# Kernel optimization log

Measured on AMD Instinct MI355X. Metric: run time of the kernel, lower is better.

Reference implementation:

```python
import jax, jax.numpy as jnp
import numpy as np

EPS = 1e-6

def rmsnorm(x, w):
    # x * rsqrt(mean(x^2, -1) + eps) * w
    ms = jnp.mean(jnp.square(x), axis=-1, keepdims=True)
    return w * (x * jax.lax.rsqrt(ms + EPS))

def setup_inputs() -> dict:
    key = jax.random.key(0)
    ks = jax.random.split(key, 10)
    B, L, T, D, R = 4, 8, 2048, 1024, 64
    h_base = jax.random.normal(ks[0], (B, T, D), dtype=jnp.float32)
    prev_states = jax.random.normal(ks[1], (B, L, T, D), dtype=jnp.float32)
    query = jax.random.normal(ks[2], (D,), dtype=jnp.float32) * 0.02
    gate = jnp.float32(0.5)
    score_w = jnp.ones((D,), dtype=jnp.float32)
    out_w = jnp.ones((D,), dtype=jnp.float32)
    qnorm_w = jnp.ones((D,), dtype=jnp.float32)
    # low-rank query projections (nn.Linear weight layout: [out, in])
    Wd = jax.random.normal(ks[3], (R, D), dtype=jnp.float32) * 0.02
    Wu = jax.random.normal(ks[4], (D, R), dtype=jnp.float32) * 0.02
    # token gate projection
    tg_w = jax.random.normal(ks[5], (1, D), dtype=jnp.float32) * 0.02
    tg_b = jnp.zeros((1,), dtype=jnp.float32)
    return {"h_base": h_base, "prev_states": prev_states, "query": query,
            "gate": gate, "score_w": score_w, "out_w": out_w,
            "qnorm_w": qnorm_w, "Wd": Wd, "Wu": Wu, "tg_w": tg_w, "tg_b": tg_b}

def reference(h_base, prev_states, query, gate, score_w, out_w, qnorm_w, Wd, Wu, tg_w, tg_b):
    sources = prev_states                              # [B,L,T,D]
    normed = rmsnorm(sources, score_w)                 # [B,L,T,D]
    # low-rank input-dependent query: q = query + up(down(qnorm(h)))
    qh = rmsnorm(h_base, qnorm_w)                      # [B,T,D]
    q = query + jnp.einsum('btr,dr->btd', jnp.einsum('btd,rd->btr', qh, Wd), Wu)
    scores = jnp.einsum('btd,bltd->blt', q, normed)    # [B,L,T]
    alpha = jax.nn.softmax(scores, axis=1)             # softmax over depth L
    delta = jnp.einsum('blt,bltd->btd', alpha, sources)
    delta = rmsnorm(delta, out_w)                      # [B,T,D]
    g = gate * jax.nn.sigmoid(h_base @ tg_w.T + tg_b)  # [B,T,1]
    out = h_base + g * delta
    return out, alpha
```

## Files before the change

### kernel.cpp

```cpp
#include <hip/hip_runtime.h>
#include <hip/hip_bf16.h>

#define D_DIM 1024
#define L_DIM 8
#define T_DIM 2048
#define B_DIM 4
#define TOKS  (B_DIM * T_DIM)
#define OUT_ELEMS ((size_t)TOKS * D_DIM)
#define EPSF 1e-6f

typedef __attribute__((ext_vector_type(8)))  short short8_t;
typedef __attribute__((ext_vector_type(16))) float f32x16_t;

__device__ __forceinline__ float wave_sum(float v) {
#pragma unroll
    for (int off = 32; off; off >>= 1) v += __shfl_xor(v, off, 64);
    return v;
}

__device__ __forceinline__ float dot4(const float4& a, const float4& b) {
    return a.x * b.x + a.y * b.y + a.z * b.z + a.w * b.w;
}

__device__ __forceinline__ unsigned short f2bf(float f) {
    union { __hip_bfloat16 h; unsigned short u; } x;
    x.h = __float2bfloat16(f);
    return x.u;
}

__device__ __forceinline__ float bf2f(unsigned short u) {
    union { unsigned int i; float f; } x;
    x.i = ((unsigned int)u) << 16;
    return x.f;
}

__global__ __launch_bounds__(256) void k_prep(const float* __restrict__ Wd,
                                              const float* __restrict__ qnw,
                                              const float* __restrict__ Wu,
                                              unsigned short* __restrict__ Wdq,
                                              unsigned short* __restrict__ Wubf) {
    int i = (blockIdx.x * 256 + threadIdx.x) * 4;
    float4 wd = *(const float4*)(Wd + i);
    float4 nv = *(const float4*)(qnw + (i & (D_DIM - 1)));
    short4 o1 = make_short4((short)f2bf(wd.x * nv.x), (short)f2bf(wd.y * nv.y),
                            (short)f2bf(wd.z * nv.z), (short)f2bf(wd.w * nv.w));
    *(short4*)(Wdq + i) = o1;
    float4 wu = *(const float4*)(Wu + i);
    short4 o2 = make_short4((short)f2bf(wu.x), (short)f2bf(wu.y),
                            (short)f2bf(wu.z), (short)f2bf(wu.w));
    *(short4*)(Wubf + i) = o2;
}

__global__ __launch_bounds__(512) void k_q(const float* __restrict__ h,
                                           const unsigned short* __restrict__ Wdq,
                                           const unsigned short* __restrict__ Wubf,
                                           const float* __restrict__ query,
                                           const float* __restrict__ score_w,
                                           unsigned short* __restrict__ qs) {
    __shared__ float c_red[8][2][16][64];
    __shared__ float ssq_red[8][32];
    __shared__ float scale_sh[32];
    __shared__ unsigned short r_sw[32 * 64];

    int tid  = threadIdx.x;
    int w    = tid >> 6;
    int lane = tid & 63;
    int t0   = blockIdx.x * 32;

    f32x16_t acc0, acc1;
#pragma unroll
    for (int r = 0; r < 16; ++r) { acc0[r] = 0.f; acc1[r] = 0.f; }

    int arow = lane & 31;
    int koff = w * 128 + (lane >> 5) * 8;
    const float* hrow = h + (size_t)(t0 + arow) * D_DIM + koff;
    const unsigned short* b0 = Wdq + (size_t)arow * D_DIM + koff;
    const unsigned short* b1 = Wdq + (size_t)(32 + arow) * D_DIM + koff;

    float ssq = 0.f;
#pragma unroll
    for (int s = 0; s < 8; ++s) {
        float4 ha = *(const float4*)(hrow + s * 16);
        float4 hb = *(const float4*)(hrow + s * 16 + 4);
        ssq += dot4(ha, ha) + dot4(hb, hb);
        short8_t af;
        af[0] = (short)f2bf(ha.x); af[1] = (short)f2bf(ha.y);
        af[2] = (short)f2bf(ha.z); af[3] = (short)f2bf(ha.w);
        af[4] = (short)f2bf(hb.x); af[5] = (short)f2bf(hb.y);
        af[6] = (short)f2bf(hb.z); af[7] = (short)f2bf(hb.w);
        short8_t bf0 = *(const short8_t*)(b0 + s * 16);
        short8_t bf1 = *(const short8_t*)(b1 + s * 16);
        acc0 = __builtin_amdgcn_mfma_f32_32x32x16_bf16(af, bf0, acc0, 0, 0, 0);
        acc1 = __builtin_amdgcn_mfma_f32_32x32x16_bf16(af, bf1, acc1, 0, 0, 0);
    }

    ssq += __shfl_xor(ssq, 32, 64);
    if (lane < 32) ssq_red[w][lane] = ssq;
#pragma unroll
    for (int r = 0; r < 16; ++r) {
        c_red[w][0][r][lane] = acc0[r];
        c_red[w][1][r][lane] = acc1[r];
    }
    __syncthreads();

    if (tid < 32) {
        float s8 = 0.f;
#pragma unroll
        for (int u = 0; u < 8; ++u) s8 += ssq_red[u][tid];
        scale_sh[tid] = rsqrtf(s8 * (1.f / D_DIM) + EPSF);
    }
    __syncthreads();

    for (int idx = tid; idx < 2048; idx += 512) {
        int nj = idx >> 10, rem = idx & 1023, reg = rem >> 6, ln = rem & 63;
        float v = 0.f;
#pragma unroll
        for (int u = 0; u < 8; ++u) v += c_red[u][nj][reg][ln];
        int tk = (reg & 3) + 8 * (reg >> 2) + 4 * (ln >> 5);
        int j  = nj * 32 + (ln & 31);
        v *= scale_sh[tk];
        int byte = (tk * 128 + j * 2) ^ ((tk & 7) << 4);
        r_sw[byte >> 1] = f2bf(v);
    }
    __syncthreads();

    short8_t afr[4];
#pragma unroll
    for (int s = 0; s < 4; ++s) {
        int tk = lane & 31;
        int k  = s * 16 + (lane >> 5) * 8;
        int byte = (tk * 128 + k * 2) ^ ((tk & 7) << 4);
        afr[s] = *(const short8_t*)(&r_sw[byte >> 1]);
    }

#pragma unroll
    for (int i = 0; i < 4; ++i) {
        int n0 = (w * 4 + i) * 32;
        int d  = n0 + (lane & 31);
        f32x16_t c;
#pragma unroll
        for (int r = 0; r < 16; ++r) c[r] = 0.f;
        const unsigned short* bb = Wubf + (size_t)d * 64 + (lane >> 5) * 8;
#pragma unroll
        for (int s = 0; s < 4; ++s) {
            short8_t bf = *(const short8_t*)(bb + s * 16);
            c = __builtin_amdgcn_mfma_f32_32x32x16_bf16(afr[s], bf, c, 0, 0, 0);
        }
        float qd  = query[d];
        float swd = score_w[d];
#pragma unroll
        for (int r = 0; r < 16; ++r) {
            int tk = (r & 3) + 8 * (r >> 2) + 4 * (lane >> 5);
            qs[(size_t)(t0 + tk) * D_DIM + d] = f2bf((qd + c[r]) * swd);
        }
    }
}

__global__ __launch_bounds__(256) void k_main(const float* __restrict__ h,
                                              const float* __restrict__ prev,
                                              const unsigned short* __restrict__ qs,
                                              const float* __restrict__ out_w,
                                              const float* __restrict__ tg_w,
                                              const float* __restrict__ gate,
                                              const float* __restrict__ tg_b,
                                              float* __restrict__ out,
                                              float* __restrict__ alpha_out) {
    __shared__ float red[16][264];
    __shared__ float fin[16];
    __shared__ float gred[4];
    __shared__ float dred[4];

    int tid = threadIdx.x, lane = tid & 63, w = tid >> 6;
    int blk = blockIdx.x;
    int b   = blk >> 11;
    int t   = blk & (T_DIM - 1);
    size_t tok = (size_t)blk;

    const float* pbase = prev + ((size_t)(b * L_DIM) * T_DIM + t) * D_DIM;
    float4 p[L_DIM];
#pragma unroll
    for (int l = 0; l < L_DIM; ++l)
        p[l] = ((const float4*)(pbase + (size_t)l * T_DIM * D_DIM))[tid];

    float4 h4 = ((const float4*)(h + tok * D_DIM))[tid];
    short4 qraw = *(const short4*)(qs + tok * D_DIM + tid * 4);
    float4 qv;
    qv.x = bf2f((unsigned short)qraw.x);
    qv.y = bf2f((unsigned short)qraw.y);
    qv.z = bf2f((unsigned short)qraw.z);
    qv.w = bf2f((unsigned short)qraw.w);
    float4 tw = ((const float4*)tg_w)[tid];

    float gp = wave_sum(dot4(h4, tw));
    if (lane == 0) gred[w] = gp;

#pragma unroll
    for (int l = 0; l < L_DIM; ++l) {
        red[l][tid]         = dot4(p[l], p[l]);
        red[l + 8][tid]     = dot4(p[l], qv);
    }
    __syncthreads();

    {
        int v = tid >> 4, seg = tid & 15;
        float s = 0.f;
#pragma unroll
        for (int i = 0; i < 16; ++i) s += red[v][seg + 16 * i];
#pragma unroll
        for (int off = 1; off < 16; off <<= 1) s += __shfl_xor(s, off, 64);
        if (seg == 0) fin[v] = s;
    }
    __syncthreads();

    float sc[L_DIM], mx = -1e30f;
#pragma unroll
    for (int l = 0; l < L_DIM; ++l) {
        sc[l] = fin[l + 8] * rsqrtf(fin[l] * (1.f / D_DIM) + EPSF);
        mx = fmaxf(mx, sc[l]);
    }
    float al[L_DIM], asum = 0.f;
#pragma unroll
    for (int l = 0; l < L_DIM; ++l) { al[l] = __expf(sc[l] - mx); asum += al[l]; }
    float inv = 1.f / asum;
#pragma unroll
    for (int l = 0; l < L_DIM; ++l) al[l] *= inv;

    float gd = gred[0] + gred[1] + gred[2] + gred[3];
    float g  = gate[0] / (1.f + __expf(-(gd + tg_b[0])));

    float4 dl = make_float4(0.f, 0.f, 0.f, 0.f);
#pragma unroll
    for (int l = 0; l < L_DIM; ++l) {
        dl.x += al[l] * p[l].x; dl.y += al[l] * p[l].y;
        dl.z += al[l] * p[l].z; dl.w += al[l] * p[l].w;
    }
    float dss = wave_sum(dot4(dl, dl));
    if (lane == 0) dred[w] = dss;
    __syncthreads();
    float dsum   = dred[0] + dred[1] + dred[2] + dred[3];
    float dscale = rsqrtf(dsum * (1.f / D_DIM) + EPSF);

    float4 ow = ((const float4*)out_w)[tid];
    float4 o;
    o.x = h4.x + g * dl.x * dscale * ow.x;
    o.y = h4.y + g * dl.y * dscale * ow.y;
    o.z = h4.z + g * dl.z * dscale * ow.z;
    o.w = h4.w + g * dl.w * dscale * ow.w;
    ((float4*)(out + tok * D_DIM))[tid] = o;

    if (tid < L_DIM)
        alpha_out[(size_t)b * (L_DIM * T_DIM) + tid * T_DIM + t] = al[tid];
}

extern "C" void kernel_launch(void* const* d_in, const int* in_sizes, int n_in,
                              void* d_out, int out_size, void* d_ws, size_t ws_size,
                              hipStream_t stream) {
    (void)in_sizes; (void)n_in; (void)out_size; (void)ws_size;
    const float* h       = (const float*)d_in[0];
    const float* prev    = (const float*)d_in[1];
    const float* query   = (const float*)d_in[2];
    const float* gate    = (const float*)d_in[3];
    const float* score_w = (const float*)d_in[4];
    const float* out_w   = (const float*)d_in[5];
    const float* qnw     = (const float*)d_in[6];
    const float* Wd      = (const float*)d_in[7];
    const float* Wu      = (const float*)d_in[8];
    const float* tg_w    = (const float*)d_in[9];
    const float* tg_b    = (const float*)d_in[10];

    float* out   = (float*)d_out;
    float* alpha = out + OUT_ELEMS;

    unsigned short* qsbuf = (unsigned short*)d_ws;
    unsigned short* Wdq   = qsbuf + OUT_ELEMS;
    unsigned short* Wubf  = Wdq + (size_t)64 * D_DIM;

    k_prep<<<64, 256, 0, stream>>>(Wd, qnw, Wu, Wdq, Wubf);
    k_q<<<TOKS / 32, 512, 0, stream>>>(h, Wdq, Wubf, query, score_w, qsbuf);
    k_main<<<TOKS, 256, 0, stream>>>(h, prev, qsbuf, out_w, tg_w, gate, tg_b, out, alpha);
}
```

Measured before the change: 91.44 us.

## Stage q output through LDS for coalesced stores; nontemporal prev loads and out stores

In k_q, the bf16 query results are packed in pairs and staged into a padded shared-memory tile that reuses the reduction buffer. Each row is then written to global memory as 16-byte chunks, replacing the scattered 2-byte stores. In k_main, the large prev_states stream is read with nontemporal loads and the output is written with nontemporal stores, so streaming data is kept from polluting the cache. This adds an extra barrier and LDS traffic in k_q, and dl/dot helpers now use native vector types.

New measurement: 90.44 us. Within noise of the previous version (-1.1%).

```diff
diff --git a/kernel.cpp b/kernel.cpp
--- a/kernel.cpp
+++ b/kernel.cpp
@@ -11,6 +11,9 @@
 
 typedef __attribute__((ext_vector_type(8)))  short short8_t;
 typedef __attribute__((ext_vector_type(16))) float f32x16_t;
+typedef __attribute__((ext_vector_type(4)))  float f32x4_t;
+
+#define QT_STRIDE 1048
 
 __device__ __forceinline__ float wave_sum(float v) {
 #pragma unroll
@@ -18,7 +21,7 @@
     return v;
 }
 
-__device__ __forceinline__ float dot4(const float4& a, const float4& b) {
+__device__ __forceinline__ float dot4v(const f32x4_t& a, const f32x4_t& b) {
     return a.x * b.x + a.y * b.y + a.z * b.z + a.w * b.w;
 }
 
@@ -57,10 +60,12 @@
                                            const float* __restrict__ query,
                                            const float* __restrict__ score_w,
                                            unsigned short* __restrict__ qs) {
-    __shared__ float c_red[8][2][16][64];
-    __shared__ float ssq_red[8][32];
-    __shared__ float scale_sh[32];
-    __shared__ unsigned short r_sw[32 * 64];
+    __shared__ __align__(16) char smem[70784];
+    float (*c_red)[2][16][64] = (float (*)[2][16][64])smem;
+    float (*ssq_red)[32]      = (float (*)[32])(smem + 65536);
+    float* scale_sh           = (float*)(smem + 66560);
+    unsigned short* r_sw      = (unsigned short*)(smem + 66688);
+    unsigned short* qt        = (unsigned short*)smem;
 
     int tid  = threadIdx.x;
     int w    = tid >> 6;
@@ -80,9 +85,9 @@
     float ssq = 0.f;
 #pragma unroll
     for (int s = 0; s < 8; ++s) {
-        float4 ha = *(const float4*)(hrow + s * 16);
-        float4 hb = *(const float4*)(hrow + s * 16 + 4);
-        ssq += dot4(ha, ha) + dot4(hb, hb);
+        f32x4_t ha = *(const f32x4_t*)(hrow + s * 16);
+        f32x4_t hb = *(const f32x4_t*)(hrow + s * 16 + 4);
+        ssq += dot4v(ha, ha) + dot4v(hb, hb);
         short8_t af;
         af[0] = (short)f2bf(ha.x); af[1] = (short)f2bf(ha.y);
         af[2] = (short)f2bf(ha.z); af[3] = (short)f2bf(ha.w);
@@ -132,6 +137,7 @@
         int byte = (tk * 128 + k * 2) ^ ((tk & 7) << 4);
         afr[s] = *(const short8_t*)(&r_sw[byte >> 1]);
     }
+    __syncthreads();
 
 #pragma unroll
     for (int i = 0; i < 4; ++i) {
@@ -151,8 +157,22 @@
 #pragma unroll
         for (int r = 0; r < 16; ++r) {
             int tk = (r & 3) + 8 * (r >> 2) + 4 * (lane >> 5);
-            qs[(size_t)(t0 + tk) * D_DIM + d] = f2bf((qd + c[r]) * swd);
+            unsigned int v = f2bf((qd + c[r]) * swd);
+            unsigned int pv = (unsigned int)__shfl_xor((int)v, 1, 64);
+            if ((lane & 1) == 0) {
+                unsigned int word = (v & 0xffffu) | (pv << 16);
+                *(unsigned int*)&qt[tk * QT_STRIDE + d] = word;
+            }
         }
+    }
+    __syncthreads();
+
+#pragma unroll
+    for (int j = 0; j < 8; ++j) {
+        int row   = tid >> 4;
+        int chunk = (tid & 15) + j * 16;
+        short8_t v = *(const short8_t*)&qt[row * QT_STRIDE + chunk * 8];
+        *(short8_t*)(qs + (size_t)(t0 + row) * D_DIM + chunk * 8) = v;
     }
 }
 
@@ -177,27 +197,27 @@
     size_t tok = (size_t)blk;
 
     const float* pbase = prev + ((size_t)(b * L_DIM) * T_DIM + t) * D_DIM;
-    float4 p[L_DIM];
+    f32x4_t p[L_DIM];
 #pragma unroll
     for (int l = 0; l < L_DIM; ++l)
-        p[l] = ((const float4*)(pbase + (size_t)l * T_DIM * D_DIM))[tid];
-
-    float4 h4 = ((const float4*)(h + tok * D_DIM))[tid];
+        p[l] = __builtin_nontemporal_load(((const f32x4_t*)(pbase + (size_t)l * T_DIM * D_DIM)) + tid);
+
+    f32x4_t h4 = ((const f32x4_t*)(h + tok * D_DIM))[tid];
     short4 qraw = *(const short4*)(qs + tok * D_DIM + tid * 4);
-    float4 qv;
+    f32x4_t qv;
     qv.x = bf2f((unsigned short)qraw.x);
     qv.y = bf2f((unsigned short)qraw.y);
     qv.z = bf2f((unsigned short)qraw.z);
     qv.w = bf2f((unsigned short)qraw.w);
-    float4 tw = ((const float4*)tg_w)[tid];
-
-    float gp = wave_sum(dot4(h4, tw));
+    f32x4_t tw = ((const f32x4_t*)tg_w)[tid];
+
+    float gp = wave_sum(dot4v(h4, tw));
     if (lane == 0) gred[w] = gp;
 
 #pragma unroll
     for (int l = 0; l < L_DIM; ++l) {
-        red[l][tid]         = dot4(p[l], p[l]);
-        red[l + 8][tid]     = dot4(p[l], qv);
+        red[l][tid]     = dot4v(p[l], p[l]);
+        red[l + 8][tid] = dot4v(p[l], qv);
     }
     __syncthreads();
 
@@ -228,25 +248,25 @@
     float gd = gred[0] + gred[1] + gred[2] + gred[3];
     float g  = gate[0] / (1.f + __expf(-(gd + tg_b[0])));
 
-    float4 dl = make_float4(0.f, 0.f, 0.f, 0.f);
+    f32x4_t dl = {0.f, 0.f, 0.f, 0.f};
 #pragma unroll
     for (int l = 0; l < L_DIM; ++l) {
         dl.x += al[l] * p[l].x; dl.y += al[l] * p[l].y;
         dl.z += al[l] * p[l].z; dl.w += al[l] * p[l].w;
     }
-    float dss = wave_sum(dot4(dl, dl));
+    float dss = wave_sum(dot4v(dl, dl));
     if (lane == 0) dred[w] = dss;
     __syncthreads();
     float dsum   = dred[0] + dred[1] + dred[2] + dred[3];
     float dscale = rsqrtf(dsum * (1.f / D_DIM) + EPSF);
 
-    float4 ow = ((const float4*)out_w)[tid];
-    float4 o;
+    f32x4_t ow = ((const f32x4_t*)out_w)[tid];
+    f32x4_t o;
     o.x = h4.x + g * dl.x * dscale * ow.x;
     o.y = h4.y + g * dl.y * dscale * ow.y;
     o.z = h4.z + g * dl.z * dscale * ow.z;
     o.w = h4.w + g * dl.w * dscale * ow.w;
-    ((float4*)(out + tok * D_DIM))[tid] = o;
+    __builtin_nontemporal_store(o, ((f32x4_t*)(out + tok * D_DIM)) + tid);
 
     if (tid < L_DIM)
         alpha_out[(size_t)b * (L_DIM * T_DIM) + tid * T_DIM + t] = al[tid];
```
